# Kernel tuning notes

Measured on AMD Instinct MI355X. Metric: run time of the kernel, lower is better.

## Reference

```python
import jax, jax.numpy as jnp
import numpy as np
import math

D_MODEL = 512
EXPAND = 2
D_INNER = EXPAND * D_MODEL          # 1024
HEADDIM = 16
NHEADS = D_INNER // HEADDIM         # 64
NGROUPS = 1
D_STATE = 16
D_CONV = 4
CHUNK = 256
CONV_DIM = D_INNER + 2 * NGROUPS * D_STATE      # 1056
D_IN_PROJ = 2 * D_INNER + 2 * NGROUPS * D_STATE + NHEADS  # 2144
EPS = 1e-5


def setup_inputs() -> dict:
    key = jax.random.key(0)
    ks = jax.random.split(key, 9)
    B, L = 2, 4096
    u = jax.random.normal(ks[0], (B, L, D_MODEL), dtype=jnp.float32)
    in_proj_w = jax.random.normal(ks[1], (D_IN_PROJ, D_MODEL), dtype=jnp.float32) * (1.0 / math.sqrt(D_MODEL))
    conv_w = jax.random.normal(ks[2], (CONV_DIM, D_CONV), dtype=jnp.float32) * (1.0 / math.sqrt(D_CONV))
    conv_b = jnp.zeros((CONV_DIM,), dtype=jnp.float32)
    # dt_bias = inverse-softplus of dt sampled log-uniform in [1e-3, 1e-1]
    dt = jnp.exp(jax.random.uniform(ks[3], (NHEADS,)) * (math.log(0.1) - math.log(0.001)) + math.log(0.001))
    dt_bias = dt + jnp.log(-jnp.expm1(-dt))
    A_log = jnp.log(jax.random.uniform(ks[4], (NHEADS,), minval=1.0, maxval=16.0))
    D_skip = jnp.ones((NHEADS,), dtype=jnp.float32)
    norm_w = jnp.ones((D_INNER,), dtype=jnp.float32)
    out_proj_w = jax.random.normal(ks[5], (D_MODEL, D_INNER), dtype=jnp.float32) * (1.0 / math.sqrt(D_INNER))
    return {"u": u, "in_proj_w": in_proj_w, "conv_w": conv_w, "conv_b": conv_b,
            "dt_bias": dt_bias, "A_log": A_log, "D_skip": D_skip,
            "norm_w": norm_w, "out_proj_w": out_proj_w}


def _segsum(x):
    # x: (..., T) -> (..., T, T) lower-triangular cumulative segment sums
    T = x.shape[-1]
    cs = jnp.cumsum(x, axis=-1)
    s = cs[..., :, None] - cs[..., None, :]
    mask = jnp.tril(jnp.ones((T, T), dtype=bool))
    return jnp.where(mask, s, -jnp.inf)


def _ssd(xdt, dA, Bm, Cm):
    # xdt: (b,l,h,p) already multiplied by dt; dA: (b,l,h); Bm,Cm: (b,l,h,n)
    b, l, h, p = xdt.shape
    n = Bm.shape[-1]
    nc = l // CHUNK
    xr = xdt.reshape(b, nc, CHUNK, h, p)
    Br = Bm.reshape(b, nc, CHUNK, h, n)
    Cr = Cm.reshape(b, nc, CHUNK, h, n)
    dAr = dA.reshape(b, nc, CHUNK, h).transpose(0, 3, 1, 2)  # (b,h,nc,c)
    A_cs = jnp.cumsum(dAr, axis=-1)
    # intra-chunk (diagonal blocks)
    Ldec = jnp.exp(_segsum(dAr))                              # (b,h,nc,c,c)
    Y_diag = jnp.einsum('bclhn,bcshn,bhcls,bcshp->bclhp', Cr, Br, Ldec, xr)
    # per-chunk final states
    decay_states = jnp.exp(A_cs[..., -1:] - A_cs)             # (b,h,nc,c)
    states = jnp.einsum('bclhn,bhcl,bclhp->bchpn', Br, decay_states, xr)
    states = jnp.concatenate([jnp.zeros_like(states[:, :1]), states], axis=1)
    chunk_sums = jnp.pad(A_cs[..., -1], ((0, 0), (0, 0), (1, 0)))  # (b,h,nc+1)
    decay_chunk = jnp.exp(_segsum(chunk_sums))                # (b,h,nc+1,nc+1)
    new_states = jnp.einsum('bhzc,bchpn->bzhpn', decay_chunk, states)
    prev_states = new_states[:, :-1]                          # (b,nc,h,p,n)
    # inter-chunk contribution
    state_decay_out = jnp.exp(A_cs)                           # (b,h,nc,c)
    Y_off = jnp.einsum('bclhn,bchpn,bhcl->bclhp', Cr, prev_states, state_decay_out)
    return (Y_diag + Y_off).reshape(b, l, h, p)


def _forward(u, in_proj_w, conv_w, conv_b, dt_bias, A_log, D_skip, norm_w, out_proj_w):
    b, l, _ = u.shape
    zxbcdt = jnp.einsum('bld,ed->ble', u, in_proj_w)
    z = zxbcdt[..., :D_INNER]
    xBC = zxbcdt[..., D_INNER:D_INNER + CONV_DIM]
    dt = zxbcdt[..., D_INNER + CONV_DIM:]
    dt = jax.nn.softplus(dt + dt_bias)                        # (b,l,h)
    # causal depthwise conv1d + silu
    xBC_t = xBC.transpose(0, 2, 1)                            # (b, conv_dim, l)
    conv_out = jax.lax.conv_general_dilated(
        xBC_t, conv_w[:, None, :], window_strides=(1,),
        padding=[(D_CONV - 1, 0)], feature_group_count=CONV_DIM,
        dimension_numbers=('NCH', 'OIH', 'NCH'))
    xBC = jax.nn.silu((conv_out + conv_b[None, :, None]).transpose(0, 2, 1))
    x = xBC[..., :D_INNER].reshape(b, l, NHEADS, HEADDIM)
    Bg = xBC[..., D_INNER:D_INNER + NGROUPS * D_STATE].reshape(b, l, NGROUPS, D_STATE)
    Cg = xBC[..., D_INNER + NGROUPS * D_STATE:].reshape(b, l, NGROUPS, D_STATE)
    hpg = NHEADS // NGROUPS
    Bm = jnp.repeat(Bg, hpg, axis=2)                          # (b,l,h,n)
    Cm = jnp.repeat(Cg, hpg, axis=2)
    A = -jnp.exp(A_log)                                       # (h,)
    dA = dt * A                                               # (b,l,h)
    y = _ssd(x * dt[..., None], dA, Bm, Cm)
    y = y + x * D_skip[None, None, :, None]
    y = y.reshape(b, l, D_INNER)
    # gated RMSNorm (norm_before_gate=False): norm(y * silu(z)) * w
    y = y * jax.nn.silu(z)
    y = y * jax.lax.rsqrt(jnp.mean(y * y, axis=-1, keepdims=True) + EPS) * norm_w
    return jnp.einsum('ble,de->bld', y, out_proj_w)


def reference(u, in_proj_w, conv_w, conv_b, dt_bias, A_log, D_skip, norm_w, out_proj_w):
    return _forward(u, in_proj_w, conv_w, conv_b, dt_bias, A_log, D_skip, norm_w, out_proj_w)
```

## Files before the change

### kernel.cpp

```cpp
#include <hip/hip_runtime.h>
#include <hip/hip_bf16.h>
#include <math.h>

#define D_MODEL   512
#define D_INNER   1024
#define NHEADS    64
#define HEADDIM   16
#define D_STATE   16
#define CONV_DIM  1056
#define D_IN_PROJ 2144
#define CHUNK     256
#define NCHUNK    16
#define BATCH     2
#define SEQ       4096
#define ROWS      (BATCH * SEQ)
#define LDZX      2176

typedef __bf16    bf16x8 __attribute__((ext_vector_type(8)));
typedef _Float16  f16x8  __attribute__((ext_vector_type(8)));
typedef float     f32x4  __attribute__((ext_vector_type(4)));
typedef float     f32x16 __attribute__((ext_vector_type(16)));
typedef unsigned short u16x8 __attribute__((ext_vector_type(8)));
typedef unsigned int   u32x4 __attribute__((ext_vector_type(4)));

__device__ __forceinline__ float softplusf(float x) {
    return (x > 20.f) ? x : log1pf(expf(x));
}
__device__ __forceinline__ float siluf(float x) {
    return x / (1.f + expf(-x));
}
__device__ __forceinline__ unsigned short f2b(float x) {
    union { __hip_bfloat16 h; unsigned short u; } cv;
    cv.h = __float2bfloat16(x);
    return cv.u;
}
__device__ __forceinline__ float b2f(unsigned short u) {
    union { float f; unsigned int i; } c;
    c.i = (unsigned int)u << 16;
    return c.f;
}
__device__ __forceinline__ void load_lds16(const unsigned short* g, unsigned short* l) {
    __builtin_amdgcn_global_load_lds(
        (const __attribute__((address_space(1))) void*)g,
        (__attribute__((address_space(3))) void*)l,
        16, 0, 0);
}

__global__ __launch_bounds__(256) void cast_all(const float* __restrict__ u,
                                                const float* __restrict__ Win,
                                                const float* __restrict__ Wout,
                                                unsigned short* __restrict__ u_bf,
                                                unsigned short* __restrict__ win_bf,
                                                unsigned short* __restrict__ wout_bf) {
    const int bid = blockIdx.x;
    u16x8 o;
    if (bid < 2048) {
        const int i = (bid * 256 + threadIdx.x) * 8;
        float4 a = *(const float4*)(u + i);
        float4 b = *(const float4*)(u + i + 4);
        o[0] = f2b(a.x); o[1] = f2b(a.y); o[2] = f2b(a.z); o[3] = f2b(a.w);
        o[4] = f2b(b.x); o[5] = f2b(b.y); o[6] = f2b(b.z); o[7] = f2b(b.w);
        *(u16x8*)(u_bf + i) = o;
    } else if (bid < 2592) {
        const int i = ((bid - 2048) * 256 + threadIdx.x) * 8;
        const int n = 2144 * 512;
        if (i + 8 <= n) {
            float4 a = *(const float4*)(Win + i);
            float4 b = *(const float4*)(Win + i + 4);
            o[0] = f2b(a.x); o[1] = f2b(a.y); o[2] = f2b(a.z); o[3] = f2b(a.w);
            o[4] = f2b(b.x); o[5] = f2b(b.y); o[6] = f2b(b.z); o[7] = f2b(b.w);
        } else {
            #pragma unroll
            for (int j = 0; j < 8; ++j) o[j] = (i + j < n) ? f2b(Win[i + j]) : (unsigned short)0;
        }
        *(u16x8*)(win_bf + i) = o;
    } else {
        const int i = ((bid - 2592) * 256 + threadIdx.x) * 8;
        float4 a = *(const float4*)(Wout + i);
        float4 b = *(const float4*)(Wout + i + 4);
        o[0] = f2b(a.x); o[1] = f2b(a.y); o[2] = f2b(a.z); o[3] = f2b(a.w);
        o[4] = f2b(b.x); o[5] = f2b(b.y); o[6] = f2b(b.z); o[7] = f2b(b.w);
        *(u16x8*)(wout_bf + i) = o;
    }
}

__global__ __launch_bounds__(256) void gemm_in(const unsigned short* __restrict__ A,
                                               const unsigned short* __restrict__ B,
                                               unsigned short* __restrict__ C16,
                                               float* __restrict__ dtsp,
                                               const float* __restrict__ dtb) {
    __shared__ unsigned short smem[16384];
    const int t    = threadIdx.x;
    const int wave = t >> 6;
    const int lane = t & 63;
    const int bid  = blockIdx.x;
    const int swz  = (bid & 7) * 136 + (bid >> 3);
    const int by   = swz / 17;
    const int bx   = swz - by * 17;
    const int bm   = by * 128;
    const int bn   = bx * 128;
    const int wr   = wave >> 1;
    const int wc   = wave & 1;

    const int srow = wave * 16 + (lane >> 2);
    const int scol = (lane & 3) * 8;
    const unsigned short* ga0 = A + (size_t)(bm + srow) * 512 + scol;
    const unsigned short* ga1 = A + (size_t)(bm + 64 + srow) * 512 + scol;
    const unsigned short* gb0 = B + (size_t)(bn + srow) * 512 + scol;
    const unsigned short* gb1 = B + (size_t)(bn + 64 + srow) * 512 + scol;

    const int fr = lane & 15;
    const int kb = (lane >> 4) * 8;

    f32x4 acc[4][4] = {};

    load_lds16(ga0, smem + wave * 512);
    load_lds16(ga1, smem + 2048 + wave * 512);
    load_lds16(gb0, smem + 8192 + wave * 512);
    load_lds16(gb1, smem + 8192 + 2048 + wave * 512);
    __syncthreads();

    int cur = 0;
    for (int it = 0; it < 16; ++it) {
        if (it + 1 < 16) {
            const int k0 = (it + 1) * 32;
            const int nb = cur ^ 1;
            load_lds16(ga0 + k0, smem + nb * 4096 + wave * 512);
            load_lds16(ga1 + k0, smem + nb * 4096 + 2048 + wave * 512);
            load_lds16(gb0 + k0, smem + 8192 + nb * 4096 + wave * 512);
            load_lds16(gb1 + k0, smem + 8192 + nb * 4096 + 2048 + wave * 512);
        }
        const unsigned short* Ab = smem + cur * 4096;
        const unsigned short* Bb = smem + 8192 + cur * 4096;
        bf16x8 af[4], bfr[4];
        #pragma unroll
        for (int m = 0; m < 4; ++m)
            af[m] = *reinterpret_cast<const bf16x8*>(&Ab[(wr * 64 + m * 16 + fr) * 32 + kb]);
        #pragma unroll
        for (int n = 0; n < 4; ++n)
            bfr[n] = *reinterpret_cast<const bf16x8*>(&Bb[(wc * 64 + n * 16 + fr) * 32 + kb]);
        #pragma unroll
        for (int m = 0; m < 4; ++m)
            #pragma unroll
            for (int n = 0; n < 4; ++n)
                acc[m][n] = __builtin_amdgcn_mfma_f32_16x16x32_bf16(af[m], bfr[n], acc[m][n], 0, 0, 0);
        __syncthreads();
        cur ^= 1;
    }

    if (bn == 2048) {
        #pragma unroll
        for (int m = 0; m < 4; ++m) {
            #pragma unroll
            for (int n = 0; n < 4; ++n) {
                const int col = bn + wc * 64 + fr + n * 16;
                if (col >= 2080 && col < 2144) {
                    const int h = col - 2080;
                    const float bias = dtb[h];
                    #pragma unroll
                    for (int j = 0; j < 4; ++j) {
                        const int row = bm + wr * 64 + ((lane >> 4) << 2) + m * 16 + j;
                        dtsp[(size_t)row * 64 + h] = softplusf(acc[m][n][j] + bias);
                    }
                }
            }
        }
    }
    #pragma unroll
    for (int m = 0; m < 4; ++m) {
        #pragma unroll
        for (int n = 0; n < 4; ++n) {
            const int lcol = wc * 64 + fr + n * 16;
            #pragma unroll
            for (int j = 0; j < 4; ++j) {
                const int lrow = wr * 64 + ((lane >> 4) << 2) + m * 16 + j;
                smem[lrow * 128 + lcol] = f2b(acc[m][n][j]);
            }
        }
    }
    __syncthreads();
    #pragma unroll
    for (int p = 0; p < 8; ++p) {
        const int r = p * 16 + (t >> 4);
        const int cl = (t & 15) * 8;
        u16x8 v = *(const u16x8*)&smem[r * 128 + cl];
        *(u16x8*)(C16 + (size_t)(bm + r) * LDZX + bn + cl) = v;
    }
}

__global__ __launch_bounds__(256) void gemm_out(const unsigned short* __restrict__ A,
                                                const unsigned short* __restrict__ B,
                                                float* __restrict__ C) {
    __shared__ unsigned short smem[12288];
    const int t    = threadIdx.x;
    const int wave = t >> 6;
    const int lane = t & 63;
    const int bm   = blockIdx.y * 128;
    const int bn   = blockIdx.x * 64;
    const int wr   = wave >> 1;
    const int wc   = wave & 1;

    const int srow = wave * 16 + (lane >> 2);
    const int scol = (lane & 3) * 8;
    const unsigned short* ga0 = A + (size_t)(bm + srow) * 1024 + scol;
    const unsigned short* ga1 = A + (size_t)(bm + 64 + srow) * 1024 + scol;
    const unsigned short* gb0 = B + (size_t)(bn + srow) * 1024 + scol;

    const int fr = lane & 15;
    const int kb = (lane >> 4) * 8;

    f32x4 acc[4][2] = {};

    load_lds16(ga0, smem + wave * 512);
    load_lds16(ga1, smem + 2048 + wave * 512);
    load_lds16(gb0, smem + 8192 + wave * 512);
    __syncthreads();

    int cur = 0;
    for (int it = 0; it < 32; ++it) {
        if (it + 1 < 32) {
            const int k0 = (it + 1) * 32;
            const int nb = cur ^ 1;
            load_lds16(ga0 + k0, smem + nb * 4096 + wave * 512);
            load_lds16(ga1 + k0, smem + nb * 4096 + 2048 + wave * 512);
            load_lds16(gb0 + k0, smem + 8192 + nb * 2048 + wave * 512);
        }
        const unsigned short* Ab = smem + cur * 4096;
        const unsigned short* Bb = smem + 8192 + cur * 2048;
        bf16x8 af[4], bfr[2];
        #pragma unroll
        for (int m = 0; m < 4; ++m)
            af[m] = *reinterpret_cast<const bf16x8*>(&Ab[(wr * 64 + m * 16 + fr) * 32 + kb]);
        #pragma unroll
        for (int n = 0; n < 2; ++n)
            bfr[n] = *reinterpret_cast<const bf16x8*>(&Bb[(wc * 32 + n * 16 + fr) * 32 + kb]);
        #pragma unroll
        for (int m = 0; m < 4; ++m)
            #pragma unroll
            for (int n = 0; n < 2; ++n)
                acc[m][n] = __builtin_amdgcn_mfma_f32_16x16x32_bf16(af[m], bfr[n], acc[m][n], 0, 0, 0);
        __syncthreads();
        cur ^= 1;
    }

    const int cr0 = bm + wr * 64 + ((lane >> 4) << 2);
    const int cc0 = bn + wc * 32 + fr;
    #pragma unroll
    for (int m = 0; m < 4; ++m)
        #pragma unroll
        for (int n = 0; n < 2; ++n)
            #pragma unroll
            for (int j = 0; j < 4; ++j)
                C[(size_t)(cr0 + m * 16 + j) * 512 + cc0 + n * 16] = acc[m][n][j];
}

__global__ void conv_silu44(const unsigned short* __restrict__ zxb, const float* __restrict__ cw,
                            const float* __restrict__ cb, unsigned short* __restrict__ xcb) {
    int idx = blockIdx.x * blockDim.x + threadIdx.x;
    if (idx >= (ROWS / 4) * (CONV_DIM / 4)) return;
    const int cq  = idx % (CONV_DIM / 4);
    const int blq = idx / (CONV_DIM / 4);
    const int bl0 = blq * 4;
    const int l0  = bl0 % SEQ;
    const int c4  = cq * 4;
    const unsigned short* base = zxb + (size_t)bl0 * LDZX + D_INNER + c4;
    float4 w0 = *(const float4*)(cw + (c4 + 0) * 4);
    float4 w1 = *(const float4*)(cw + (c4 + 1) * 4);
    float4 w2 = *(const float4*)(cw + (c4 + 2) * 4);
    float4 w3 = *(const float4*)(cw + (c4 + 3) * 4);
    float4 bb = *(const float4*)(cb + c4);
    float4 in[7];
    #pragma unroll
    for (int k = 0; k < 7; ++k) {
        const int off = k - 3;
        if (l0 == 0 && k < 3) {
            in[k] = make_float4(0.f, 0.f, 0.f, 0.f);
        } else {
            ushort4 uu = *(const ushort4*)(base + (long)off * LDZX);
            in[k] = make_float4(b2f(uu.x), b2f(uu.y), b2f(uu.z), b2f(uu.w));
        }
    }
    #pragma unroll
    for (int r = 0; r < 4; ++r) {
        ushort4 o;
        o.x = f2b(siluf(bb.x + w0.x * in[r].x + w0.y * in[r + 1].x + w0.z * in[r + 2].x + w0.w * in[r + 3].x));
        o.y = f2b(siluf(bb.y + w1.x * in[r].y + w1.y * in[r + 1].y + w1.z * in[r + 2].y + w1.w * in[r + 3].y));
        o.z = f2b(siluf(bb.z + w2.x * in[r].z + w2.y * in[r + 1].z + w2.z * in[r + 2].z + w2.w * in[r + 3].z));
        o.w = f2b(siluf(bb.w + w3.x * in[r].w + w3.y * in[r + 1].w + w3.z * in[r + 2].w + w3.w * in[r + 3].w));
        *(ushort4*)(xcb + (size_t)(bl0 + r) * CONV_DIM + c4) = o;
    }
}

__global__ __launch_bounds__(256, 4) void ssd_chunk(const unsigned short* __restrict__ xcb,
                                                    const float* __restrict__ dtsp,
                                                    const float* __restrict__ A_log,
                                                    unsigned short* __restrict__ ypre16,
                                                    float* __restrict__ states,
                                                    float* __restrict__ csb,
                                                    float* __restrict__ csum) {
    __shared__ _Float16 Bb[256][16];
    __shared__ _Float16 Cb[256][16];
    __shared__ _Float16 Xt[16][264];
    __shared__ _Float16 Bt[16][264];
    __shared__ float csL[256];
    __shared__ __align__(16) _Float16 decL[256];
    __shared__ float wsumL[4];

    const int bid = blockIdx.x;
    const int h = bid & 63;
    const int c = (bid >> 6) & 15;
    const int b = bid >> 10;
    const int t = threadIdx.x;
    const int wv = t >> 6;
    const int lane = t & 63;
    const int fr = lane & 15;
    const int hi = lane >> 4;
    const int l31 = lane & 31;
    const int hi5 = lane >> 5;
    const int row = b * SEQ + c * CHUNK + t;

    float Ah  = -__expf(A_log[h]);
    float dtv = dtsp[(size_t)row * NHEADS + h];
    float val = dtv * Ah;
    #pragma unroll
    for (int off = 1; off < 64; off <<= 1) {
        float o = __shfl_up(val, off, 64);
        if (lane >= off) val += o;
    }
    if (lane == 63) wsumL[wv] = val;
    __syncthreads();
    float pre = 0.f, cl = 0.f;
    #pragma unroll
    for (int w2 = 0; w2 < 4; ++w2) {
        float s = wsumL[w2];
        if (w2 < wv) pre += s;
        cl += s;
    }
    float cst = val + pre;
    csL[t] = cst;
    csb[(size_t)bid * 256 + t] = cst;
    if (t == 0) csum[(b * 64 + h) * 16 + c] = cl;
    decL[t] = (_Float16)__expf(cl - cst);

    const unsigned short* xrow = xcb + (size_t)row * CONV_DIM;
    u16x8 braw0 = *(const u16x8*)(xrow + D_INNER);
    u16x8 braw1 = *(const u16x8*)(xrow + D_INNER + 8);
    u16x8 craw0 = *(const u16x8*)(xrow + D_INNER + D_STATE);
    u16x8 craw1 = *(const u16x8*)(xrow + D_INNER + D_STATE + 8);
    u16x8 xraw0 = *(const u16x8*)(xrow + h * HEADDIM);
    u16x8 xraw1 = *(const u16x8*)(xrow + h * HEADDIM + 8);
    float bv[16], cv[16], xv[16];
    #pragma unroll
    for (int n = 0; n < 8; ++n) {
        bv[n] = b2f(braw0[n]); bv[8 + n] = b2f(braw1[n]);
        cv[n] = b2f(craw0[n]); cv[8 + n] = b2f(craw1[n]);
        xv[n] = b2f(xraw0[n]); xv[8 + n] = b2f(xraw1[n]);
    }
    {
        f16x8 pk;
        #pragma unroll
        for (int n = 0; n < 8; ++n) pk[n] = (_Float16)cv[n];
        *(f16x8*)&Cb[t][0] = pk;
        #pragma unroll
        for (int n = 0; n < 8; ++n) pk[n] = (_Float16)cv[8 + n];
        *(f16x8*)&Cb[t][8] = pk;
        #pragma unroll
        for (int n = 0; n < 8; ++n) pk[n] = (_Float16)bv[n];
        *(f16x8*)&Bb[t][0] = pk;
        #pragma unroll
        for (int n = 0; n < 8; ++n) pk[n] = (_Float16)bv[8 + n];
        *(f16x8*)&Bb[t][8] = pk;
    }
    #pragma unroll
    for (int n = 0; n < 16; ++n) {
        Bt[n][t] = (_Float16)bv[n];
        Xt[n][t] = (_Float16)(xv[n] * dtv);
    }
    __syncthreads();

    const int browbase = b * SEQ + c * CHUNK;
    const f32x16 z16 = {};

    #pragma unroll
    for (int halfi = 0; halfi < 2; ++halfi) {
        const int rt = (halfi == 0) ? wv : 7 - wv;
        const int t0 = rt * 32;
        const float cs_t = csL[t0 + l31];
        const f16x8 cfrag = *(const f16x8*)&Cb[t0 + l31][hi5 * 8];
        f32x16 yacc = {};
        for (int sb = 0; sb <= rt; ++sb) {
            const int s0 = sb * 32;
            f16x8 bfrag = *(const f16x8*)&Bb[s0 + l31][hi5 * 8];
            f32x16 sp = __builtin_amdgcn_mfma_f32_32x32x16_f16(bfrag, cfrag, z16, 0, 0, 0);
            const bool diag = (sb == rt);
            unsigned int D[8];
            #pragma unroll
            for (int j = 0; j < 8; ++j) {
                const int q0 = 2 * j;
                const int sr0 = (q0 & 3) + 8 * (q0 >> 2) + 4 * hi5;
                float p0 = sp[q0] * __expf(cs_t - csL[s0 + sr0]);
                float p1 = sp[q0 + 1] * __expf(cs_t - csL[s0 + sr0 + 1]);
                if (diag) {
                    p0 = (sr0 <= l31) ? p0 : 0.f;
                    p1 = (sr0 + 1 <= l31) ? p1 : 0.f;
                }
                D[j] = __builtin_bit_cast(unsigned int, __builtin_amdgcn_cvt_pkrtz(p0, p1));
            }
            unsigned int pD[8];
            #pragma unroll
            for (int j = 0; j < 8; ++j) pD[j] = (unsigned int)__shfl_xor((int)D[j], 32, 64);
            u32x4 fa;
            fa[0] = hi5 ? pD[2] : D[0];
            fa[1] = hi5 ? pD[3] : D[1];
            fa[2] = hi5 ? D[2] : pD[0];
            fa[3] = hi5 ? D[3] : pD[1];
            f16x8 pf0 = __builtin_bit_cast(f16x8, fa);
            f16x8 xf0 = *(const f16x8*)&Xt[fr][s0 + hi5 * 8];
            yacc = __builtin_amdgcn_mfma_f32_32x32x16_f16(pf0, xf0, yacc, 0, 0, 0);
            fa[0] = hi5 ? pD[6] : D[4];
            fa[1] = hi5 ? pD[7] : D[5];
            fa[2] = hi5 ? D[6] : pD[4];
            fa[3] = hi5 ? D[7] : pD[5];
            f16x8 pf1 = __builtin_bit_cast(f16x8, fa);
            f16x8 xf1 = *(const f16x8*)&Xt[fr][s0 + 16 + hi5 * 8];
            yacc = __builtin_amdgcn_mfma_f32_32x32x16_f16(pf1, xf1, yacc, 0, 0, 0);
        }
        if (l31 < 16) {
            #pragma unroll
            for (int q = 0; q < 16; ++q) {
                const int tr = t0 + (q & 3) + 8 * (q >> 2) + 4 * hi5;
                ypre16[(size_t)(browbase + tr) * D_INNER + h * HEADDIM + l31] = f2b(yacc[q]);
            }
        }
    }

    __syncthreads();
    float* stpart = (float*)&Cb[0][0];
    const int r0w = wv * 64;
    f32x4 stacc = {};
    #pragma unroll
    for (int kt = 0; kt < 2; ++kt) {
        const int sbase = r0w + kt * 32 + hi * 8;
        f16x8 xa = *(const f16x8*)&Xt[fr][sbase];
        f16x8 dd = *(const f16x8*)&decL[sbase];
        xa = xa * dd;
        f16x8 bb2 = *(const f16x8*)&Bt[fr][sbase];
        stacc = __builtin_amdgcn_mfma_f32_16x16x32_f16(xa, bb2, stacc, 0, 0, 0);
    }
    #pragma unroll
    for (int j = 0; j < 4; ++j)
        stpart[wv * 256 + (hi * 4 + j) * 16 + fr] = stacc[j];
    __syncthreads();
    {
        const int p = t >> 4, n = t & 15;
        float st = stpart[0 * 256 + p * 16 + n] + stpart[1 * 256 + p * 16 + n]
                 + stpart[2 * 256 + p * 16 + n] + stpart[3 * 256 + p * 16 + n];
        states[(size_t)bid * 256 + t] = st;
    }
}

__global__ __launch_bounds__(256) void ssd_rec(const float* __restrict__ states,
                                               const float* __restrict__ csum,
                                               float* __restrict__ prevst) {
    __shared__ float dec[16];
    const int bh = blockIdx.x;
    const int b = bh >> 6, h = bh & 63;
    const int t = threadIdx.x;
    if (t < 16) dec[t] = __expf(csum[bh * 16 + t]);
    float sv[16];
    #pragma unroll
    for (int c = 0; c < NCHUNK; ++c)
        sv[c] = states[((size_t)((b * 16 + c) * 64 + h)) * 256 + t];
    __syncthreads();
    float run = 0.f;
    #pragma unroll
    for (int c = 0; c < NCHUNK; ++c) {
        prevst[((size_t)((b * 16 + c) * 64 + h)) * 256 + t] = run;
        run = run * dec[c] + sv[c];
    }
}

__global__ __launch_bounds__(512, 4) void ssd_off_norm(const unsigned short* __restrict__ xcb,
                                                       const unsigned short* __restrict__ zxb,
                                                       const unsigned short* __restrict__ ypre16,
                                                       const float* __restrict__ prevst,
                                                       const float* __restrict__ csb,
                                                       const float* __restrict__ Dskip,
                                                       const float* __restrict__ normw,
                                                       unsigned short* __restrict__ yout) {
    __shared__ float Cs[16][16];
    __shared__ float csS[64][16];
    __shared__ float nw[1024];
    __shared__ float Dn[64];
    __shared__ float red[16][8];

    const int blk = blockIdx.x;
    const int bc = blk >> 4;
    const int rb = blk & 15;
    const int r0 = rb * 16;
    const int b = bc >> 4, c = bc & 15;
    const int brow0 = b * SEQ + c * CHUNK;
    const int t = threadIdx.x;
    const int ch0 = t * 2;
    const int h = ch0 >> 4;
    const int p0 = ch0 & 15;
    const int wv = t >> 6;
    const int lane = t & 63;

    if (t < 256) *(float4*)&nw[t * 4] = *(const float4*)(normw + t * 4);
    else if (t < 320) Dn[t - 256] = Dskip[t - 256];
    if (t < 64) {
        int r = t >> 2, n4 = (t & 3) * 4;
        ushort4 uu = *(const ushort4*)(xcb + (size_t)(brow0 + r0 + r) * CONV_DIM
                                       + D_INNER + D_STATE + n4);
        Cs[r][n4 + 0] = b2f(uu.x); Cs[r][n4 + 1] = b2f(uu.y);
        Cs[r][n4 + 2] = b2f(uu.z); Cs[r][n4 + 3] = b2f(uu.w);
    }
    #pragma unroll
    for (int i = t; i < 1024; i += 512) {
        int r = i & 15, hh = i >> 4;
        csS[hh][r] = csb[(size_t)(bc * 64 + hh) * 256 + r0 + r];
    }

    float ps[2][16];
    {
        const float* pbase = prevst + (size_t)(bc * 64 + h) * 256 + p0 * 16;
        #pragma unroll
        for (int n4 = 0; n4 < 16; n4 += 4) {
            *(float4*)&ps[0][n4] = *(const float4*)(pbase + n4);
            *(float4*)&ps[1][n4] = *(const float4*)(pbase + 16 + n4);
        }
    }
    __syncthreads();

    const float d = Dn[h];
    const float nw0 = nw[ch0], nw1 = nw[ch0 + 1];

    float g0r[16], g1r[16];
    #pragma unroll
    for (int r = 0; r < 16; ++r) {
        const size_t grow = (size_t)(brow0 + r0 + r);
        ushort2 yu = *(const ushort2*)(ypre16 + grow * D_INNER + ch0);
        ushort2 xu = *(const ushort2*)(xcb + grow * CONV_DIM + ch0);
        ushort2 zu = *(const ushort2*)(zxb + grow * LDZX + ch0);
        float sdo = __expf(csS[h][r]);
        float off0 = 0.f, off1 = 0.f;
        #pragma unroll
        for (int n = 0; n < 16; ++n) {
            float cn = Cs[r][n];
            off0 += cn * ps[0][n];
            off1 += cn * ps[1][n];
        }
        float g0 = (b2f(yu.x) + sdo * off0 + b2f(xu.x) * d) * siluf(b2f(zu.x));
        float g1 = (b2f(yu.y) + sdo * off1 + b2f(xu.y) * d) * siluf(b2f(zu.y));
        g0r[r] = g0; g1r[r] = g1;
        float s = g0 * g0 + g1 * g1;
        #pragma unroll
        for (int o = 32; o > 0; o >>= 1) s += __shfl_down(s, o, 64);
        if (lane == 0) red[r][wv] = s;
    }
    __syncthreads();
    #pragma unroll
    for (int r = 0; r < 16; ++r) {
        const size_t grow = (size_t)(brow0 + r0 + r);
        float tot = 0.f;
        #pragma unroll
        for (int w2 = 0; w2 < 8; ++w2) tot += red[r][w2];
        float rstd = rsqrtf(tot * (1.f / (float)D_INNER) + 1e-5f);
        ushort2 o2;
        o2.x = f2b(g0r[r] * rstd * nw0);
        o2.y = f2b(g1r[r] * rstd * nw1);
        *(ushort2*)(yout + grow * D_INNER + ch0) = o2;
    }
}

extern "C" void kernel_launch(void* const* d_in, const int* in_sizes, int n_in,
                              void* d_out, int out_size, void* d_ws, size_t ws_size,
                              hipStream_t stream) {
    const float* u     = (const float*)d_in[0];
    const float* Win   = (const float*)d_in[1];
    const float* cw    = (const float*)d_in[2];
    const float* cb    = (const float*)d_in[3];
    const float* dtb   = (const float*)d_in[4];
    const float* Alog  = (const float*)d_in[5];
    const float* Dsk   = (const float*)d_in[6];
    const float* normw = (const float*)d_in[7];
    const float* Wout  = (const float*)d_in[8];
    float* out = (float*)d_out;

    float* ws = (float*)d_ws;
    unsigned short* zxb = (unsigned short*)ws;
    float* dtsp   = ws + 8912896;
    float* csb    = dtsp + 524288;
    float* st     = csb + 524288;
    float* pst    = st + 524288;
    float* csum   = pst + 524288;
    unsigned short* ypre16 = (unsigned short*)(csum + 2048);
    unsigned short* xcb    = (unsigned short*)((float*)ypre16 + 4194304);
    unsigned short* yn_bf  = (unsigned short*)((float*)xcb + 4325376);
    unsigned short* u_bf   = (unsigned short*)((float*)yn_bf + 2097152);
    unsigned short* win_bf  = (unsigned short*)((float*)u_bf + 2097152);
    unsigned short* wout_bf = (unsigned short*)((float*)win_bf + 557056);

    cast_all<<<2848, 256, 0, stream>>>(u, Win, Wout, u_bf, win_bf, wout_bf);

    gemm_in<<<1088, 256, 0, stream>>>(u_bf, win_bf, zxb, dtsp, dtb);

    conv_silu44<<<(ROWS / 4) * (CONV_DIM / 4) / 256, 256, 0, stream>>>(zxb, cw, cb, xcb);
    ssd_chunk<<<BATCH * NCHUNK * NHEADS, 256, 0, stream>>>(xcb, dtsp, Alog, ypre16, st, csb, csum);
    ssd_rec<<<BATCH * NHEADS, 256, 0, stream>>>(st, csum, pst);
    ssd_off_norm<<<512, 512, 0, stream>>>(xcb, zxb, ypre16, pst, csb, Dsk, normw, yn_bf);

    gemm_out<<<dim3(8, 64), 256, 0, stream>>>(yn_bf, wout_bf, out);
}
```

Baseline: 143.2 us.

## Double K-tile depth to 64 with XOR-swizzled LDS layout in both GEMMs

Both projection GEMMs now stage 64-wide K slices per iteration instead of 32, which halves the number of barrier-separated main-loop iterations. The LDS tile rows are stored with an XOR swizzle on 16-byte slots, so the row-strided fragment reads avoid bank conflicts. LDS use doubles per block, which could reduce occupancy, and the epilogue of gemm_in reuses smem with a 128-wide stride that still fits.

```diff
diff --git a/kernel.cpp b/kernel.cpp
--- a/kernel.cpp
+++ b/kernel.cpp
@@ -89,7 +89,7 @@
                                                unsigned short* __restrict__ C16,
                                                float* __restrict__ dtsp,
                                                const float* __restrict__ dtb) {
-    __shared__ unsigned short smem[16384];
+    __shared__ unsigned short smem[32768];
     const int t    = threadIdx.x;
     const int wave = t >> 6;
     const int lane = t & 63;
@@ -102,50 +102,59 @@
     const int wr   = wave >> 1;
     const int wc   = wave & 1;
 
-    const int srow = wave * 16 + (lane >> 2);
-    const int scol = (lane & 3) * 8;
-    const unsigned short* ga0 = A + (size_t)(bm + srow) * 512 + scol;
-    const unsigned short* ga1 = A + (size_t)(bm + 64 + srow) * 512 + scol;
-    const unsigned short* gb0 = B + (size_t)(bn + srow) * 512 + scol;
-    const unsigned short* gb1 = B + (size_t)(bn + 64 + srow) * 512 + scol;
-
     const int fr = lane & 15;
     const int kb = (lane >> 4) * 8;
 
     f32x4 acc[4][4] = {};
 
-    load_lds16(ga0, smem + wave * 512);
-    load_lds16(ga1, smem + 2048 + wave * 512);
-    load_lds16(gb0, smem + 8192 + wave * 512);
-    load_lds16(gb1, smem + 8192 + 2048 + wave * 512);
-    __syncthreads();
-
-    int cur = 0;
-    for (int it = 0; it < 16; ++it) {
-        if (it + 1 < 16) {
-            const int k0 = (it + 1) * 32;
-            const int nb = cur ^ 1;
-            load_lds16(ga0 + k0, smem + nb * 4096 + wave * 512);
-            load_lds16(ga1 + k0, smem + nb * 4096 + 2048 + wave * 512);
-            load_lds16(gb0 + k0, smem + 8192 + nb * 4096 + wave * 512);
-            load_lds16(gb1 + k0, smem + 8192 + nb * 4096 + 2048 + wave * 512);
-        }
-        const unsigned short* Ab = smem + cur * 4096;
-        const unsigned short* Bb = smem + 8192 + cur * 4096;
-        bf16x8 af[4], bfr[4];
-        #pragma unroll
-        for (int m = 0; m < 4; ++m)
-            af[m] = *reinterpret_cast<const bf16x8*>(&Ab[(wr * 64 + m * 16 + fr) * 32 + kb]);
-        #pragma unroll
-        for (int n = 0; n < 4; ++n)
-            bfr[n] = *reinterpret_cast<const bf16x8*>(&Bb[(wc * 64 + n * 16 + fr) * 32 + kb]);
-        #pragma unroll
-        for (int m = 0; m < 4; ++m)
-            #pragma unroll
-            for (int n = 0; n < 4; ++n)
-                acc[m][n] = __builtin_amdgcn_mfma_f32_16x16x32_bf16(af[m], bfr[n], acc[m][n], 0, 0, 0);
+    auto stage = [&](int it) {
+        const int k0 = it * 64;
+        unsigned short* dst = smem + (it & 1) * 16384;
+        #pragma unroll
+        for (int q = 0; q < 4; ++q) {
+            const int p = q * 256 + t;
+            const int r = p >> 3;
+            const int sl = (p & 7) ^ (r & 7);
+            load_lds16(A + (size_t)(bm + r) * 512 + k0 + sl * 8, dst + p * 8);
+        }
+        #pragma unroll
+        for (int q = 0; q < 4; ++q) {
+            const int p = q * 256 + t;
+            const int r = p >> 3;
+            const int sl = (p & 7) ^ (r & 7);
+            load_lds16(B + (size_t)(bn + r) * 512 + k0 + sl * 8, dst + 8192 + p * 8);
+        }
+    };
+
+    stage(0);
+    __syncthreads();
+
+    for (int it = 0; it < 8; ++it) {
+        if (it + 1 < 8) stage(it + 1);
+        const unsigned short* Ab = smem + (it & 1) * 16384;
+        const unsigned short* Bb = Ab + 8192;
+        #pragma unroll
+        for (int kk = 0; kk < 2; ++kk) {
+            const int c0 = kk * 32 + kb;
+            const int s0 = c0 >> 3;
+            bf16x8 af[4], bfr[4];
+            #pragma unroll
+            for (int m = 0; m < 4; ++m) {
+                const int R = wr * 64 + m * 16 + fr;
+                af[m] = *reinterpret_cast<const bf16x8*>(&Ab[R * 64 + ((s0 ^ (R & 7)) << 3)]);
+            }
+            #pragma unroll
+            for (int n = 0; n < 4; ++n) {
+                const int R = wc * 64 + n * 16 + fr;
+                bfr[n] = *reinterpret_cast<const bf16x8*>(&Bb[R * 64 + ((s0 ^ (R & 7)) << 3)]);
+            }
+            #pragma unroll
+            for (int m = 0; m < 4; ++m)
+                #pragma unroll
+                for (int n = 0; n < 4; ++n)
+                    acc[m][n] = __builtin_amdgcn_mfma_f32_16x16x32_bf16(af[m], bfr[n], acc[m][n], 0, 0, 0);
+        }
         __syncthreads();
-        cur ^= 1;
     }
 
     if (bn == 2048) {
@@ -191,7 +200,7 @@
 __global__ __launch_bounds__(256) void gemm_out(const unsigned short* __restrict__ A,
                                                 const unsigned short* __restrict__ B,
                                                 float* __restrict__ C) {
-    __shared__ unsigned short smem[12288];
+    __shared__ unsigned short smem[24576];
     const int t    = threadIdx.x;
     const int wave = t >> 6;
     const int lane = t & 63;
@@ -200,47 +209,59 @@
     const int wr   = wave >> 1;
     const int wc   = wave & 1;
 
-    const int srow = wave * 16 + (lane >> 2);
-    const int scol = (lane & 3) * 8;
-    const unsigned short* ga0 = A + (size_t)(bm + srow) * 1024 + scol;
-    const unsigned short* ga1 = A + (size_t)(bm + 64 + srow) * 1024 + scol;
-    const unsigned short* gb0 = B + (size_t)(bn + srow) * 1024 + scol;
-
     const int fr = lane & 15;
     const int kb = (lane >> 4) * 8;
 
     f32x4 acc[4][2] = {};
 
-    load_lds16(ga0, smem + wave * 512);
-    load_lds16(ga1, smem + 2048 + wave * 512);
-    load_lds16(gb0, smem + 8192 + wave * 512);
-    __syncthreads();
-
-    int cur = 0;
-    for (int it = 0; it < 32; ++it) {
-        if (it + 1 < 32) {
-            const int k0 = (it + 1) * 32;
-            const int nb = cur ^ 1;
-            load_lds16(ga0 + k0, smem + nb * 4096 + wave * 512);
-            load_lds16(ga1 + k0, smem + nb * 4096 + 2048 + wave * 512);
-            load_lds16(gb0 + k0, smem + 8192 + nb * 2048 + wave * 512);
-        }
-        const unsigned short* Ab = smem + cur * 4096;
-        const unsigned short* Bb = smem + 8192 + cur * 2048;
-        bf16x8 af[4], bfr[2];
-        #pragma unroll
-        for (int m = 0; m < 4; ++m)
-            af[m] = *reinterpret_cast<const bf16x8*>(&Ab[(wr * 64 + m * 16 + fr) * 32 + kb]);
-        #pragma unroll
-        for (int n = 0; n < 2; ++n)
-            bfr[n] = *reinterpret_cast<const bf16x8*>(&Bb[(wc * 32 + n * 16 + fr) * 32 + kb]);
-        #pragma unroll
-        for (int m = 0; m < 4; ++m)
-            #pragma unroll
-            for (int n = 0; n < 2; ++n)
-                acc[m][n] = __builtin_amdgcn_mfma_f32_16x16x32_bf16(af[m], bfr[n], acc[m][n], 0, 0, 0);
+    auto stage = [&](int it) {
+        const int k0 = it * 64;
+        unsigned short* dst = smem + (it & 1) * 12288;
+        #pragma unroll
+        for (int q = 0; q < 4; ++q) {
+            const int p = q * 256 + t;
+            const int r = p >> 3;
+            const int sl = (p & 7) ^ (r & 7);
+            load_lds16(A + (size_t)(bm + r) * 1024 + k0 + sl * 8, dst + p * 8);
+        }
+        #pragma unroll
+        for (int q = 0; q < 2; ++q) {
+            const int p = q * 256 + t;
+            const int r = p >> 3;
+            const int sl = (p & 7) ^ (r & 7);
+            load_lds16(B + (size_t)(bn + r) * 1024 + k0 + sl * 8, dst + 8192 + p * 8);
+        }
+    };
+
+    stage(0);
+    __syncthreads();
+
+    for (int it = 0; it < 16; ++it) {
+        if (it + 1 < 16) stage(it + 1);
+        const unsigned short* Ab = smem + (it & 1) * 12288;
+        const unsigned short* Bb = Ab + 8192;
+        #pragma unroll
+        for (int kk = 0; kk < 2; ++kk) {
+            const int c0 = kk * 32 + kb;
+            const int s0 = c0 >> 3;
+            bf16x8 af[4], bfr[2];
+            #pragma unroll
+            for (int m = 0; m < 4; ++m) {
+                const int R = wr * 64 + m * 16 + fr;
+                af[m] = *reinterpret_cast<const bf16x8*>(&Ab[R * 64 + ((s0 ^ (R & 7)) << 3)]);
+            }
+            #pragma unroll
+            for (int n = 0; n < 2; ++n) {
+                const int R = wc * 32 + n * 16 + fr;
+                bfr[n] = *reinterpret_cast<const bf16x8*>(&Bb[R * 64 + ((s0 ^ (R & 7)) << 3)]);
+            }
+            #pragma unroll
+            for (int m = 0; m < 4; ++m)
+                #pragma unroll
+                for (int n = 0; n < 2; ++n)
+                    acc[m][n] = __builtin_amdgcn_mfma_f32_16x16x32_bf16(af[m], bfr[n], acc[m][n], 0, 0, 0);
+        }
         __syncthreads();
-        cur ^= 1;
     }
 
     const int cr0 = bm + wr * 64 + ((lane >> 4) << 2);
```

After: 144.7 us. Within noise of the previous version (+1.0%).
